# Kernel tuning notes

Hardware: AMD Instinct MI355X
Metric: run time of the kernel (lower is better)

## Reference

```python
import jax, jax.numpy as jnp
import numpy as np
from math import factorial

NODES = 40000      # number of nodes
EDGES = 640000     # number of edges (avg degree 16)
MUL = 8            # multiplicity of each irrep in hidden (8x0e+8x1e+8x2e)
NB = 16            # radial basis size (radial_neurons[0])
MAXR = 3.0         # max_radius
NSPECIES = 8
DEG = 16.0         # num_neighbors normalization
R8 = 1.0 / np.sqrt(8.0)

# ---------- real Clebsch-Gordan coefficients (precomputed with numpy) ----------
def _clebsch(j1, m1, j2, m2, j3, m3):
    f = factorial
    if m1 + m2 != m3:
        return 0.0
    pref = ((2*j3+1) * f(j3+j1-j2) * f(j3-j1+j2) * f(j1+j2-j3) / f(j1+j2+j3+1)) ** 0.5
    pref *= (f(j3+m3)*f(j3-m3)*f(j1-m1)*f(j1+m1)*f(j2-m2)*f(j2+m2)) ** 0.5
    lo = max(0, j2-j3-m1, j1-j3+m2)
    hi = min(j1+j2-j3, j1-m1, j2+m2)
    s = 0.0
    for k in range(lo, hi+1):
        s += (-1)**k / (f(k)*f(j1+j2-j3-k)*f(j1-m1-k)*f(j2+m2-k)*f(j3-j2+m1+k)*f(j3-j1-m2+k))
    return pref * s

def _U(l):
    # complex -> real spherical-harmonic change of basis (rows: real m, cols: complex m)
    U = np.zeros((2*l+1, 2*l+1), dtype=complex)
    s2 = 2 ** -0.5
    for m in range(-l, l+1):
        if m > 0:
            U[m+l, m+l] = (-1)**m * s2; U[m+l, -m+l] = s2
        elif m == 0:
            U[l, l] = 1.0
        else:
            U[m+l, m+l] = 1j*s2; U[m+l, -m+l] = -1j*((-1)**m)*s2
    return U

def _real_cg(l1, l2, l3):
    C = np.zeros((2*l1+1, 2*l2+1, 2*l3+1))
    for m1 in range(-l1, l1+1):
        for m2 in range(-l2, l2+1):
            m3 = m1 + m2
            if abs(m3) <= l3:
                C[m1+l1, m2+l2, m3+l3] = _clebsch(l1, m1, l2, m2, l3, m3)
    T = np.einsum('am,bn,co,mno->abc', _U(l1).conj(), _U(l2).conj(), _U(l3), C)
    R = T.imag if np.abs(T.imag).max() > np.abs(T.real).max() else T.real
    return jnp.asarray(R.astype(np.float32))

PATHS = [(0,0,0),(0,1,1),(0,2,2),(1,0,1),(1,1,0),(1,1,1),(1,1,2),
         (1,2,1),(1,2,2),(2,0,2),(2,1,1),(2,1,2),(2,2,0),(2,2,1),(2,2,2)]
CG = {p: _real_cg(*p) for p in PATHS}
NIN = {0: 3.0, 1: 6.0, 2: 6.0}  # fan-in path counts per output l in hidden convs

# ---------- irrep feature layout: [.., 72] = 8x0e | 8x1e | 8x2e ----------
def _split(h):
    lead = h.shape[:-1]
    return (h[..., :MUL],
            h[..., MUL:4*MUL].reshape(lead + (MUL, 3)),
            h[..., 4*MUL:].reshape(lead + (MUL, 5)))

def _merge(s, v, t):
    lead = s.shape[:-1]
    return jnp.concatenate([s, v.reshape(lead + (3*MUL,)), t.reshape(lead + (5*MUL,))], -1)

def _act(h):
    # e3nn Activation: silu on 0e scalars, identity on l>0
    s, v, t = _split(h)
    return _merge(jax.nn.silu(s), v, t)

def _radial(emb, w1, b1, w2, b2):
    return jax.nn.silu(emb @ w1 + b1) @ w2 + b2

def _sh(u):
    # component-normalized real spherical harmonics l=0,1,2 of unit vectors u [E,3]
    x, y, z = u[:, 0], u[:, 1], u[:, 2]
    c15 = np.sqrt(15.0); c5 = np.sqrt(5.0); c3 = np.sqrt(3.0)
    y1 = jnp.stack([y, z, x], -1) * c3
    y2 = jnp.stack([c15*x*y, c15*y*z, 0.5*c5*(3*z*z - 1.0), c15*x*z, 0.5*c15*(x*x - y*y)], -1)
    return jnp.concatenate([jnp.ones_like(x)[:, None], y1, y2], -1)

def _soft_onehot(r):
    # e3nn soft_one_hot_linspace, basis='smooth_finite', cutoff=True
    values = jnp.linspace(0.0, MAXR, NB + 2)[1:-1]
    step = MAXR / (NB + 1)
    d = (r[:, None] - values) / step
    inside = jnp.abs(d) < 1.0
    dd = jnp.where(inside, d, 0.0)
    f = jnp.exp(-1.0 / (1.0 + dd)) * jnp.exp(-1.0 / (1.0 - dd))
    return 1.14136 * np.exp(2.0) * jnp.where(inside, f, 0.0)

def _tp_first(hs, sh, w):
    # uvu TP: 8x0e (x) SH(1x0e+1x1e+1x2e) -> hidden; hs [E,8], sh [E,9], w [E,3,8]
    m_s = w[:, 0] * hs * sh[:, :1]
    m_v = w[:, 1][..., None] * hs[..., None] * sh[:, None, 1:4]
    m_t = w[:, 2][..., None] * hs[..., None] * sh[:, None, 4:9]
    return _merge(m_s, m_v, m_t)

def _tp_uuu(h1, h2, w):
    # depthwise (uuu) CG tensor product hidden (x) hidden -> hidden; w [E,15,8]
    s1, v1, t1 = _split(h1); s2, v2, t2 = _split(h2)
    a = {0: s1[..., None], 1: v1, 2: t1}
    b = {0: s2[..., None], 1: v2, 2: t2}
    out = {0: 0.0, 1: 0.0, 2: 0.0}
    for p, (l1, l2, l3) in enumerate(PATHS):
        out[l3] = out[l3] + w[:, p, :, None] * jnp.einsum('eci,ecj,ijk->eck', a[l1], b[l2], CG[(l1, l2, l3)])
    return _merge(out[0][..., 0] / np.sqrt(NIN[0]), out[1] / np.sqrt(NIN[1]), out[2] / np.sqrt(NIN[2]))

def _lin_hidden(h, lin):
    # irrep-wise linear self-connection, lin [3,8,8]
    s, v, t = _split(h)
    return _merge(s @ lin[0] * R8,
                  jnp.einsum('ncm,cd->ndm', v, lin[1]) * R8,
                  jnp.einsum('ncm,cd->ndm', t, lin[2]) * R8)

def _model(x, edge_index, edge_vec, embed_w, lin0, lin1, lin2, out_w,
           r0_w1, r0_b1, r0_w2, r0_b2, r1_w1, r1_b1, r1_w2, r1_b2,
           r2_w1, r2_b1, r2_w2, r2_b2):
    src, dst = edge_index[0], edge_index[1]
    h = embed_w[x]                                   # [N, 8] scalar node feats
    r = jnp.sqrt(jnp.sum(edge_vec**2, -1) + 1e-12)
    emb = _soft_onehot(r)                            # [E, 16]
    hb_sh = _sh(edge_vec / r[:, None])               # [E, 9]
    rdeg = 1.0 / np.sqrt(DEG)
    # conv 0 + activation
    w = _radial(emb, r0_w1, r0_b1, r0_w2, r0_b2).reshape(-1, 3, MUL)
    m = _tp_first(h[src], hb_sh, w)                  # [E, 72]
    agg = jax.ops.segment_sum(m, dst, num_segments=NODES) * rdeg
    h = _act(agg.at[:, :MUL].add((h @ lin0) * R8))
    hb = _act(m)
    # convs 1..2 + activation
    for (w1, b1, w2, b2, lin) in ((r1_w1, r1_b1, r1_w2, r1_b2, lin1),
                                  (r2_w1, r2_b1, r2_w2, r2_b2, lin2)):
        w = _radial(emb, w1, b1, w2, b2).reshape(-1, 15, MUL)
        m = _tp_uuu(h[src], hb, w)
        agg = jax.ops.segment_sum(m, dst, num_segments=NODES) * rdeg
        h = _act(_lin_hidden(h, lin) + agg)
        hb = _act(m)
    # output FullyConnectedTensorProduct(h, h) -> 8x0e (paths l(x)l->0)
    s, v, t = _split(h)
    i0 = s[:, :, None] * s[:, None, :]
    i1 = jnp.einsum('nim,njm->nij', v, v) / np.sqrt(3.0)
    i2 = jnp.einsum('nim,njm->nij', t, t) / np.sqrt(5.0)
    out = (jnp.einsum('nij,ijk->nk', i0, out_w[0])
           + jnp.einsum('nij,ijk->nk', i1, out_w[1])
           + jnp.einsum('nij,ijk->nk', i2, out_w[2])) / np.sqrt(3.0 * MUL * MUL)
    return out

def setup_inputs() -> dict:
    key = jax.random.key(0)
    ks = jax.random.split(key, 16)
    inp = {}
    inp['x'] = jax.random.randint(ks[0], (NODES,), 0, NSPECIES)
    inp['edge_index'] = jax.random.randint(ks[1], (2, EDGES), 0, NODES)
    inp['edge_vec'] = jax.random.normal(ks[2], (EDGES, 3), dtype=jnp.float32)
    inp['embed_w'] = jax.random.normal(ks[3], (NSPECIES, MUL), dtype=jnp.float32)
    inp['lin0'] = jax.random.normal(ks[4], (MUL, MUL), dtype=jnp.float32)
    inp['lin1'] = jax.random.normal(ks[5], (3, MUL, MUL), dtype=jnp.float32)
    inp['lin2'] = jax.random.normal(ks[6], (3, MUL, MUL), dtype=jnp.float32)
    inp['out_w'] = jax.random.normal(ks[7], (3, MUL, MUL, MUL), dtype=jnp.float32)
    for i, (name, od) in enumerate((('r0', 3*MUL), ('r1', 15*MUL), ('r2', 15*MUL))):
        k1, k2 = jax.random.split(ks[8+i])
        inp[name+'_w1'] = jax.random.normal(k1, (NB, 64), dtype=jnp.float32) / np.sqrt(NB)
        inp[name+'_b1'] = jnp.zeros((64,), dtype=jnp.float32)
        inp[name+'_w2'] = jax.random.normal(k2, (64, od), dtype=jnp.float32) / 8.0
        inp[name+'_b2'] = jnp.zeros((od,), dtype=jnp.float32)
    return inp

def reference(x, edge_index, edge_vec, embed_w, lin0, lin1, lin2, out_w,
              r0_w1, r0_b1, r0_w2, r0_b2, r1_w1, r1_b1, r1_w2, r1_b2,
              r2_w1, r2_b1, r2_w2, r2_b2):
    return _model(x, edge_index, edge_vec, embed_w, lin0, lin1, lin2, out_w,
                  r0_w1, r0_b1, r0_w2, r0_b2, r1_w1, r1_b1, r1_w2, r1_b2,
                  r2_w1, r2_b1, r2_w2, r2_b2)
```

## Files before the change

### kernel.cpp

```cpp
#include <hip/hip_runtime.h>

#define NODES 40000
#define EDGES 640000

typedef float f32x2v __attribute__((ext_vector_type(2)));
typedef float f32x4v __attribute__((ext_vector_type(4)));
typedef short short8v __attribute__((ext_vector_type(8)));

__device__ __forceinline__ float silu_f(float x) { return x / (1.0f + __expf(-x)); }
__device__ __forceinline__ f32x2v mk2(float a, float b) { f32x2v r; r[0] = a; r[1] = b; return r; }

__device__ __forceinline__ void tp_uuu2(const f32x2v* wv,
                                        f32x2v as, const f32x2v* av, const f32x2v* at,
                                        f32x2v bs, const f32x2v* bv, const f32x2v* bt,
                                        f32x2v& ms, f32x2v* mv, f32x2v* mt)
{
    const float CR = 0.70710678f;
    const float K1 = 0.31622777f;
    const float K3 = 0.54772256f;
    const float KA = 0.40824829f;
    const float KB = 0.70710678f;
    const float KC = 0.81649658f;
    const float L4 = 0.63245553f;
    const float G2 = 0.53452248f;
    const float G1 = 0.26726124f;
    const float HH = 0.46291005f;

    f32x2v os = {0.f, 0.f};
    f32x2v ov0 = {0.f, 0.f}, ov1 = {0.f, 0.f}, ov2 = {0.f, 0.f};
    f32x2v ot0 = {0.f, 0.f}, ot1 = {0.f, 0.f}, ot2 = {0.f, 0.f};
    f32x2v ot3 = {0.f, 0.f}, ot4 = {0.f, 0.f};

    os += wv[0] * as * bs;
    ov0 += wv[1] * as * bv[0]; ov1 += wv[1] * as * bv[1]; ov2 += wv[1] * as * bv[2];
    ot0 += wv[2] * as * bt[0]; ot1 += wv[2] * as * bt[1]; ot2 += wv[2] * as * bt[2];
    ot3 += wv[2] * as * bt[3]; ot4 += wv[2] * as * bt[4];
    ov0 += wv[3] * av[0] * bs; ov1 += wv[3] * av[1] * bs; ov2 += wv[3] * av[2] * bs;
    os += wv[4] * (-0.57735027f) * (av[0]*bv[0] + av[1]*bv[1] + av[2]*bv[2]);
    ov0 += wv[5] * CR * (av[1]*bv[2] - av[2]*bv[1]);
    ov1 += wv[5] * CR * (av[2]*bv[0] - av[0]*bv[2]);
    ov2 += wv[5] * CR * (av[0]*bv[1] - av[1]*bv[0]);
    ot0 += wv[6] * CR * (av[2]*bv[0] + av[0]*bv[2]);
    ot1 += wv[6] * CR * (av[0]*bv[1] + av[1]*bv[0]);
    ot2 += wv[6] * 0.40824829f * (2.f*av[1]*bv[1] - av[2]*bv[2] - av[0]*bv[0]);
    ot3 += wv[6] * CR * (av[2]*bv[1] + av[1]*bv[2]);
    ot4 += wv[6] * CR * (av[2]*bv[2] - av[0]*bv[0]);
    ov0 += wv[7] * (-K3*av[1]*bt[1] + K1*av[0]*bt[2] - K3*av[2]*bt[0] + K3*av[0]*bt[4]);
    ov1 += wv[7] * (-2.f*K1*av[1]*bt[2] - K3*av[2]*bt[3] - K3*av[0]*bt[1]);
    ov2 += wv[7] * (-K3*av[1]*bt[3] + K1*av[2]*bt[2] - K3*av[0]*bt[0] - K3*av[2]*bt[4]);
    ot0 += wv[8] * ( KC*av[1]*bt[4] - KA*av[2]*bt[3] + KA*av[0]*bt[1]);
    ot1 += wv[8] * ( KA*av[1]*bt[3] - KB*av[2]*bt[2] - KA*av[0]*bt[0] - KA*av[2]*bt[4]);
    ot2 += wv[8] * ( KB*av[2]*bt[1] - KB*av[0]*bt[3]);
    ot3 += wv[8] * (-KA*av[1]*bt[1] + KB*av[0]*bt[2] + KA*av[2]*bt[0] - KA*av[0]*bt[4]);
    ot4 += wv[8] * (-KC*av[1]*bt[0] + KA*av[2]*bt[1] + KA*av[0]*bt[3]);
    ot0 += wv[9] * at[0] * bs; ot1 += wv[9] * at[1] * bs; ot2 += wv[9] * at[2] * bs;
    ot3 += wv[9] * at[3] * bs; ot4 += wv[9] * at[4] * bs;
    ov0 += wv[10] * (-K3*bv[1]*at[1] + K1*bv[0]*at[2] - K3*bv[2]*at[0] + K3*bv[0]*at[4]);
    ov1 += wv[10] * (-2.f*K1*bv[1]*at[2] - K3*bv[2]*at[3] - K3*bv[0]*at[1]);
    ov2 += wv[10] * (-K3*bv[1]*at[3] + K1*bv[2]*at[2] - K3*bv[0]*at[0] - K3*bv[2]*at[4]);
    ot0 -= wv[11] * ( KC*bv[1]*at[4] - KA*bv[2]*at[3] + KA*bv[0]*at[1]);
    ot1 -= wv[11] * ( KA*bv[1]*at[3] - KB*bv[2]*at[2] - KA*bv[0]*at[0] - KA*bv[2]*at[4]);
    ot2 -= wv[11] * ( KB*bv[2]*at[1] - KB*bv[0]*at[3]);
    ot3 -= wv[11] * (-KA*bv[1]*at[1] + KB*bv[0]*at[2] + KA*bv[2]*at[0] - KA*bv[0]*at[4]);
    ot4 -= wv[11] * (-KC*bv[1]*at[0] + KA*bv[2]*at[1] + KA*bv[0]*at[3]);
    os += wv[12] * 0.44721360f * (at[0]*bt[0] + at[1]*bt[1] + at[2]*bt[2] + at[3]*bt[3] + at[4]*bt[4]);
    ov0 += wv[13] * ( K1*(at[0]*bt[1] - at[1]*bt[0]) + K3*(at[3]*bt[2] - at[2]*bt[3]) + K1*(at[4]*bt[3] - at[3]*bt[4]) );
    ov1 += wv[13] * ( L4*(at[0]*bt[4] - at[4]*bt[0]) + K1*(at[1]*bt[3] - at[3]*bt[1]) );
    ov2 += wv[13] * ( K1*(at[3]*bt[0] - at[0]*bt[3]) + K3*(at[2]*bt[1] - at[1]*bt[2]) + K1*(at[4]*bt[1] - at[1]*bt[4]) );
    ot0 += wv[14] * ( G2*(at[2]*bt[0] + at[0]*bt[2]) - HH*(at[1]*bt[3] + at[3]*bt[1]) );
    ot1 += wv[14] * (-HH*(at[3]*bt[0] + at[0]*bt[3]) + HH*(at[1]*bt[4] + at[4]*bt[1]) - G1*(at[2]*bt[1] + at[1]*bt[2]) );
    ot2 += wv[14] * ( G2*(at[0]*bt[0] + at[4]*bt[4] - at[2]*bt[2]) - G1*(at[1]*bt[1] + at[3]*bt[3]) );
    ot3 += wv[14] * (-HH*(at[1]*bt[0] + at[0]*bt[1]) - HH*(at[3]*bt[4] + at[4]*bt[3]) - G1*(at[2]*bt[3] + at[3]*bt[2]) );
    ot4 += wv[14] * ( G2*(at[2]*bt[4] + at[4]*bt[2]) + HH*(at[1]*bt[1] - at[3]*bt[3]) );

    ms = os * 0.57735027f;
    mv[0] = ov0 * 0.40824829f; mv[1] = ov1 * 0.40824829f; mv[2] = ov2 * 0.40824829f;
    mt[0] = ot0 * 0.40824829f; mt[1] = ot1 * 0.40824829f; mt[2] = ot2 * 0.40824829f;
    mt[3] = ot3 * 0.40824829f; mt[4] = ot4 * 0.40824829f;
}

__global__ void deg_kernel(const int* __restrict__ eidx, int* __restrict__ deg)
{
    int e = blockIdx.x * 256 + threadIdx.x;
    if (e < EDGES) atomicAdd(&deg[eidx[EDGES + e]], 1);
}

__launch_bounds__(1024)
__global__ void scan_kernel(const int* __restrict__ deg, int* __restrict__ off,
                            int* __restrict__ cursor)
{
    __shared__ int part[1024];
    const int t = threadIdx.x;
    const int base = t * 40;
    int v[40];
    if (t < 1000) {
        const int4* p4 = (const int4*)(deg + base);
        #pragma unroll
        for (int i = 0; i < 10; ++i) {
            int4 q = p4[i];
            v[4 * i + 0] = q.x; v[4 * i + 1] = q.y;
            v[4 * i + 2] = q.z; v[4 * i + 3] = q.w;
        }
    } else {
        #pragma unroll
        for (int i = 0; i < 40; ++i) v[i] = 0;
    }
    int loc[40];
    int s = 0;
    #pragma unroll
    for (int i = 0; i < 40; ++i) { loc[i] = s; s += v[i]; }
    part[t] = s;
    __syncthreads();
    for (int d = 1; d < 1024; d <<= 1) {
        int vv = (t >= d) ? part[t - d] : 0;
        __syncthreads();
        part[t] += vv;
        __syncthreads();
    }
    int tb = (t == 0) ? 0 : part[t - 1];
    if (t < 1000) {
        #pragma unroll
        for (int i = 0; i < 40; ++i) {
            off[base + i] = tb + loc[i];
            cursor[base + i] = tb + loc[i];
        }
    }
    if (t == 1023) off[NODES] = part[1023];
}

__global__ void build_kernel(const int* __restrict__ eidx, const float* __restrict__ ev,
                             int* __restrict__ cursor,
// ... 53 lines not shown
            float4 wb = *(const float4*)&w1[i * 64 + jb + 4];
            #pragma unroll
            for (int el = 0; el < 4; ++el) {
                float evv = emb_s[(egp * 4 + el) * 17 + i];
                acc2[el][0] += evv * wa.x; acc2[el][1] += evv * wa.y;
                acc2[el][2] += evv * wa.z; acc2[el][3] += evv * wa.w;
                acc2[el][4] += evv * wb.x; acc2[el][5] += evv * wb.y;
                acc2[el][6] += evv * wb.z; acc2[el][7] += evv * wb.w;
            }
        }
        #pragma unroll
        for (int el = 0; el < 4; ++el)
            #pragma unroll
            for (int k = 0; k < 8; ++k)
                hid_s[(egp * 4 + el) * 68 + jb + k] = silu_f(acc2[el][k]);
    }
    __syncthreads();

    const int c = tid & 7, g = (tid >> 3) & 7, wv_ = tid >> 6;
    float wacc[3][4];
    #pragma unroll
    for (int p = 0; p < 3; ++p) {
        float bb = b2[p * 8 + c];
        #pragma unroll
        for (int q = 0; q < 4; ++q) wacc[p][q] = bb;
    }
    for (int jb = 0; jb < 64; jb += 4) {
        float4 h4[4];
        #pragma unroll
        for (int q = 0; q < 4; ++q)
            h4[q] = *(const float4*)&hid_s[(wv_ * 32 + q * 8 + g) * 68 + jb];
        #pragma unroll
        for (int p = 0; p < 3; ++p) {
            float4 w4 = *(const float4*)&w2t[(p * 8 + c) * 68 + jb];
            #pragma unroll
            for (int q = 0; q < 4; ++q)
                wacc[p][q] += h4[q].x * w4.x + h4[q].y * w4.y + h4[q].z * w4.z + h4[q].w * w4.w;
        }
    }

    const int ebase = wv_ * 32 + g;
    #pragma unroll
    for (int q = 0; q < 4; ++q) {
        const int sl = e0 + ebase + 8 * q;
        const int sn = (int)((unsigned)srcs[sl] & 0xffffu);
        float hs = embw[xs[sn] * 8 + c];
        float* me = mbuf + (size_t)sl * 72;
        me[c]      = wacc[0][q] * hs;
        me[8 + c]  = wacc[1][q] * hs;
        me[16 + c] = wacc[2][q] * hs;
    }
}

__launch_bounds__(256, 3)
__global__ void tp_edge(const float* __restrict__ evp, const int* __restrict__ srcs,
                        const float* __restrict__ h,
                        const float* __restrict__ w1, const float* __restrict__ b1,
                        const float* __restrict__ w2, const float* __restrict__ b2,
                        float* __restrict__ mbuf, float* __restrict__ agg,
                        const int writeM, const int compactB)
{
    __shared__ float ws_t[120 * 68];
    __shared__ unsigned short hid_s[128 * 64];
    __shared__ int dst_s[66];
    float* emb_s = ws_t;

    const int tid = threadIdx.x;
    const int e0 = blockIdx.x * 128;

    for (int idx = tid; idx < 2048; idx += 256) {
        int e = idx >> 4, i = idx & 15;
        const float* ep = evp + (size_t)(e0 + e) * 3;
        float ex = ep[0], ey = ep[1], ez = ep[2];
        float r = sqrtf(ex * ex + ey * ey + ez * ez + 1e-12f);
        float d = r * (17.0f / 3.0f) - (float)(i + 1);
        float f = 0.0f;
        if (fabsf(d) < 1.0f) f = 8.433572869f * __expf(-2.0f / (1.0f - d * d));
        emb_s[e * 17 + i] = f;
    }
    __syncthreads();

    {
        const int egp = tid >> 3;
        const int jb = (tid & 7) * 8;
        f32x2v acc2[2][8];
        #pragma unroll
        for (int pr = 0; pr < 2; ++pr)
            #pragma unroll
            for (int k = 0; k < 8; ++k) { float bb = b1[jb + k]; acc2[pr][k] = mk2(bb, bb); }
        #pragma unroll
        for (int i = 0; i < 16; ++i) {
            float4 wa = *(const float4*)&w1[i * 64 + jb];
            float4 wb = *(const float4*)&w1[i * 64 + jb + 4];
            #pragma unroll
            for (int pr = 0; pr < 2; ++pr) {
                f32x2v evv = mk2(emb_s[(egp * 4 + 2 * pr) * 17 + i],
                                 emb_s[(egp * 4 + 2 * pr + 1) * 17 + i]);
                acc2[pr][0] += evv * wa.x; acc2[pr][1] += evv * wa.y;
                acc2[pr][2] += evv * wa.z; acc2[pr][3] += evv * wa.w;
                acc2[pr][4] += evv * wb.x; acc2[pr][5] += evv * wb.y;
                acc2[pr][6] += evv * wb.z; acc2[pr][7] += evv * wb.w;
            }
        }
        #pragma unroll
        for (int pr = 0; pr < 2; ++pr) {
            #pragma unroll
            for (int u = 0; u < 2; ++u) {
                unsigned int us[8];
                #pragma unroll
                for (int k = 0; k < 8; ++k) {
                    unsigned int b = __float_as_uint(silu_f(acc2[pr][k][u]));
                    b += 0x7fffu + ((b >> 16) & 1u);
                    us[k] = b >> 16;
                }
                uint4 pk;
                pk.x = us[0] | (us[1] << 16);
                pk.y = us[2] | (us[3] << 16);
                pk.z = us[4] | (us[5] << 16);
                pk.w = us[6] | (us[7] << 16);
                int rr = egp * 4 + 2 * pr + u;
                *(uint4*)&hid_s[rr * 64 + (jb ^ ((rr & 7) << 3))] = pk;
            }
        }
    }
    __syncthreads();

    const int l  = tid & 63;
    const int wq = tid >> 6;
    const int lr = l & 15;
    const int lg = l >> 4;

    short8v bhi[2][2], blo[2][2];
    #pragma unroll
    for (int n2 = 0; n2 < 2; ++n2) {
        int col  = (2 * wq + n2) * 16 + lr;
        int colc = col < 120 ? col : 119;
        #pragma unroll
        for (int ks = 0; ks < 2; ++ks) {
            short8v hv, lv;
            #pragma unroll
            for (int j = 0; j < 8; ++j) {
                int k = ks * 32 + lg * 8 + j;
                float v = w2[k * 120 + colc];
                if (col >= 120) v = 0.0f;
                unsigned bb = __float_as_uint(v);
                unsigned rh = bb + 0x7fffu + ((bb >> 16) & 1u);
                float hf = __uint_as_float((rh >> 16) << 16);
                unsigned bl = __float_as_uint(v - hf);
                bl += 0x7fffu + ((bl >> 16) & 1u);
                hv[j] = (short)(rh >> 16);
                lv[j] = (short)(bl >> 16);
            }
            bhi[n2][ks] = hv;
            blo[n2][ks] = lv;
        }
    }

    const int c = tid & 7, g = (tid >> 3) & 7, wv_ = tid >> 6;
    const int ebh = wv_ * 16 + g;

    #pragma unroll
    for (int half = 0; half < 2; ++half) {
        #pragma unroll
        for (int mm = 0; mm < 4; ++mm) {
            int e  = 64 * half + 16 * mm + lr;
            int sw = (e & 7) << 3;
            short8v a0 = *(const short8v*)&hid_s[e * 64 + ((lg * 8) ^ sw)];
            short8v a1 = *(const short8v*)&hid_s[e * 64 + ((32 + lg * 8) ^ sw)];
            #pragma unroll
            for (int n2 = 0; n2 < 2; ++n2) {
                int col = (2 * wq + n2) * 16 + lr;
                float bias = (col < 120) ? b2[col] : 0.0f;
                f32x4v acc;
                acc[0] = bias; acc[1] = bias; acc[2] = bias; acc[3] = bias;
                acc = __builtin_amdgcn_mfma_f32_16x16x32_bf16(a0, bhi[n2][0], acc, 0, 0, 0);
                acc = __builtin_amdgcn_mfma_f32_16x16x32_bf16(a1, bhi[n2][1], acc, 0, 0, 0);
                acc = __builtin_amdgcn_mfma_f32_16x16x32_bf16(a0, blo[n2][0], acc, 0, 0, 0);
                acc = __builtin_amdgcn_mfma_f32_16x16x32_bf16(a1, blo[n2][1], acc, 0, 0, 0);
                if (col < 120)
                    *(f32x4v*)&ws_t[col * 68 + 16 * mm + lg * 4] = acc;
            }
        }
        __syncthreads();

        {
            const int eA = e0 + 64 * half + ebh;
            const int eB = eA + 8;
            const unsigned pkA = (unsigned)srcs[eA], pkB = (unsigned)srcs[eB];
            const int snA = (int)(pkA & 0xffffu), snB = (int)(pkB & 0xffffu);
            const float* hn0 = h + (size_t)snA * 72 + c * 9;
            const float* hn1 = h + (size_t)snB * 72 + c * 9;

            f32x2v as = mk2(hn0[0], hn1[0]);
            f32x2v av[3], at[5], bv[3], bt[5], bs;
            #pragma unroll
            for (int i = 0; i < 3; ++i) av[i] = mk2(hn0[1 + i], hn1[1 + i]);
            #pragma unroll
            for (int i = 0; i < 5; ++i) at[i] = mk2(hn0[4 + i], hn1[4 + i]);

            if (compactB) {
                float w0A = mbuf[(size_t)eA * 72 + c];
                float w1A = mbuf[(size_t)eA * 72 + 8 + c];
                float w2A = mbuf[(size_t)eA * 72 + 16 + c];
                float w0B = mbuf[(size_t)eB * 72 + c];
                float w1B = mbuf[(size_t)eB * 72 + 8 + c];
                float w2B = mbuf[(size_t)eB * 72 + 16 + c];
                const float* epA = evp + (size_t)eA * 3;
                const float* epB = evp + (size_t)eB * 3;
                float exA = epA[0], eyA = epA[1], ezA = epA[2];
                float exB = epB[0], eyB = epB[1], ezB = epB[2];
                float rA = sqrtf(exA * exA + eyA * eyA + ezA * ezA + 1e-12f);
                float rB = sqrtf(exB * exB + eyB * eyB + ezB * ezB + 1e-12f);
                float iA = 1.0f / rA, iB = 1.0f / rB;
                float xA = exA * iA, yA = eyA * iA, zA = ezA * iA;
                float xB = exB * iB, yB = eyB * iB, zB = ezB * iB;
                const float c3 = 1.7320508f, c15 = 3.8729833f, c5 = 2.2360680f;
                bs = mk2(silu_f(w0A), silu_f(w0B));
                bv[0] = mk2(w1A * (c3 * yA), w1B * (c3 * yB));
                bv[1] = mk2(w1A * (c3 * zA), w1B * (c3 * zB));
                bv[2] = mk2(w1A * (c3 * xA), w1B * (c3 * xB));
                bt[0] = mk2(w2A * (c15 * xA * yA), w2B * (c15 * xB * yB));
                bt[1] = mk2(w2A * (c15 * yA * zA), w2B * (c15 * yB * zB));
                bt[2] = mk2(w2A * (0.5f * c5 * (3.f * zA * zA - 1.f)),
                            w2B * (0.5f * c5 * (3.f * zB * zB - 1.f)));
                bt[3] = mk2(w2A * (c15 * xA * zA), w2B * (c15 * xB * zB));
                bt[4] = mk2(w2A * (0.5f * c15 * (xA * xA - yA * yA)),
                            w2B * (0.5f * c15 * (xB * xB - yB * yB)));
            } else {
                const float* me0 = mbuf + (size_t)eA * 72 + c * 9;
                const float* me1 = mbuf + (size_t)eB * 72 + c * 9;
                bs = mk2(silu_f(me0[0]), silu_f(me1[0]));
                #pragma unroll
                for (int i = 0; i < 3; ++i) bv[i] = mk2(me0[1 + i], me1[1 + i]);
                #pragma unroll
                for (int i = 0; i < 5; ++i) bt[i] = mk2(me0[4 + i], me1[4 + i]);
            }

            f32x2v wvv[15];
            #pragma unroll
            for (int p = 0; p < 15; ++p)
                wvv[p] = mk2(ws_t[(p * 8 + c) * 68 + ebh],
                             ws_t[(p * 8 + c) * 68 + ebh + 8]);

            f32x2v ms, mv[3], mt[5];
            tp_uuu2(wvv, as, av, at, bs, bv, bt, ms, mv, mt);

            if (writeM) {
                float* mo0 = mbuf + (size_t)eA * 72 + c * 9;
                float* mo1 = mbuf + (size_t)eB * 72 + c * 9;
                mo0[0] = ms[0]; mo1[0] = ms[1];
                #pragma unroll
                for (int i = 0; i < 3; ++i) { mo0[1 + i] = mv[i][0]; mo1[1 + i] = mv[i][1]; }
                #pragma unroll
                for (int i = 0; i < 5; ++i) { mo0[4 + i] = mt[i][0]; mo1[4 + i] = mt[i][1]; }
            }

            if (tid <= 64) {
                int gs = e0 + 64 * half + tid;
                dst_s[tid] = (gs < EDGES) ? (int)((unsigned)srcs[gs] >> 16) : -1;
            }
            __syncthreads();

            float* m_s = ws_t;
            const int lA = ebh, lB = ebh + 8;
            m_s[lA * 72 + c * 9] = ms[0]; m_s[lB * 72 + c * 9] = ms[1];
            #pragma unroll
            for (int i = 0; i < 3; ++i) {
                m_s[lA * 72 + c * 9 + 1 + i] = mv[i][0];
                m_s[lB * 72 + c * 9 + 1 + i] = mv[i][1];
            }
            #pragma unroll
            for (int i = 0; i < 5; ++i) {
                m_s[lA * 72 + c * 9 + 4 + i] = mt[i][0];
                m_s[lB * 72 + c * 9 + 4 + i] = mt[i][1];
            }
            __syncthreads();

            if (tid < 216) {
                const int seg  = tid / 72;
                const int comp = tid - seg * 72;
                const int p0 = (seg == 0) ? 0  : ((seg == 1) ? 22 : 43);
                const int p1 = (seg == 0) ? 22 : ((seg == 1) ? 43 : 64);
                float sum = 0.f;
                int cur = dst_s[p0];
                for (int p = p0; p < p1; ++p) {
                    sum += m_s[p * 72 + comp];
                    int nxt = dst_s[p + 1];
                    if (nxt != cur) {
                        atomicAdd(&agg[(size_t)cur * 72 + comp], sum);
                        sum = 0.f; cur = nxt;
                    }
                }
                if (cur >= 0) atomicAdd(&agg[(size_t)cur * 72 + comp], sum);
            }
        }
        if (half == 0) __syncthreads();
    }
}

__global__ void node0(const int* __restrict__ xs, const float* __restrict__ embw,
                      const float* __restrict__ lin0, const float* __restrict__ mbuf,
                      const float* __restrict__ evp,
                      const int* __restrict__ off, float* __restrict__ h)
{
    int idx = blockIdx.x * 256 + threadIdx.x;
    int n = idx >> 3, c = idx & 7;
    int xb = xs[n] * 8;
    float dot = 0.f;
    #pragma unroll
    for (int d = 0; d < 8; ++d) dot += embw[xb + d] * lin0[d * 8 + c];

    float an[9];
    #pragma unroll
    for (int i = 0; i < 9; ++i) an[i] = 0.f;
    const float c3 = 1.7320508f, c15 = 3.8729833f, c5 = 2.2360680f;
    const int beg = off[n], end = off[n + 1];
    for (int p = beg; p < end; ++p) {
        float w0 = mbuf[(size_t)p * 72 + c];
        float w1 = mbuf[(size_t)p * 72 + 8 + c];
        float w2 = mbuf[(size_t)p * 72 + 16 + c];
        const float* ep = evp + (size_t)p * 3;
        float ex = ep[0], ey = ep[1], ez = ep[2];
        float r = sqrtf(ex * ex + ey * ey + ez * ez + 1e-12f);
        float inv = 1.0f / r;
        float x = ex * inv, y = ey * inv, z = ez * inv;
        an[0] += w0;
        an[1] += w1 * (c3 * y);
        an[2] += w1 * (c3 * z);
        an[3] += w1 * (c3 * x);
        an[4] += w2 * (c15 * x * y);
        an[5] += w2 * (c15 * y * z);
        an[6] += w2 * (0.5f * c5 * (3.f * z * z - 1.f));
        an[7] += w2 * (c15 * x * z);
        an[8] += w2 * (0.5f * c15 * (x * x - y * y));
    }

    float* hn = h + (size_t)n * 72 + c * 9;
    hn[0] = silu_f(an[0] * 0.25f + dot * 0.35355339f);
    #pragma unroll
    for (int i = 1; i < 9; ++i) hn[i] = an[i] * 0.25f;
}

__global__ void node12(const float* __restrict__ hin, const float* __restrict__ lin,
                       const float* __restrict__ agg, float* __restrict__ hout)
{
    int idx = blockIdx.x * 256 + threadIdx.x;
    int n = idx >> 3, d = idx & 7;

    float an[9];
// ... 145 lines not shown
```

Measured before the change: 666.4 us.

## Split radial weight GEMM into two column halves to shrink LDS and raise occupancy

The radial MLP output (120 columns) is now computed in two 64-column halves. Tensor-product paths 0-7 are evaluated on the first half before the second half overwrites the same smaller shared buffer, and paths 8-14 then run on the second half. This shrinks the shared weight tile from 120x68 to 64x72 floats so the launch bound can rise from 3 to 4 blocks per CU. The cost is two extra block barriers per half-iteration and partial accumulators that stay live across the split, which adds register pressure.

```diff
diff --git a/kernel.cpp b/kernel.cpp
--- a/kernel.cpp
+++ b/kernel.cpp
@@ -10,12 +10,39 @@
 __device__ __forceinline__ float silu_f(float x) { return x / (1.0f + __expf(-x)); }
 __device__ __forceinline__ f32x2v mk2(float a, float b) { f32x2v r; r[0] = a; r[1] = b; return r; }
 
-__device__ __forceinline__ void tp_uuu2(const f32x2v* wv,
-                                        f32x2v as, const f32x2v* av, const f32x2v* at,
-                                        f32x2v bs, const f32x2v* bv, const f32x2v* bt,
-                                        f32x2v& ms, f32x2v* mv, f32x2v* mt)
+__device__ __forceinline__ void tp_paths07(const f32x2v* wv,
+        f32x2v as, const f32x2v* av, const f32x2v* at,
+        f32x2v bs, const f32x2v* bv, const f32x2v* bt,
+        f32x2v& os, f32x2v* ov, f32x2v* ot)
 {
     const float CR = 0.70710678f;
+    const float K1 = 0.31622777f;
+    const float K3 = 0.54772256f;
+
+    os += wv[0] * as * bs;
+    ov[0] += wv[1] * as * bv[0]; ov[1] += wv[1] * as * bv[1]; ov[2] += wv[1] * as * bv[2];
+    ot[0] += wv[2] * as * bt[0]; ot[1] += wv[2] * as * bt[1]; ot[2] += wv[2] * as * bt[2];
+    ot[3] += wv[2] * as * bt[3]; ot[4] += wv[2] * as * bt[4];
+    ov[0] += wv[3] * av[0] * bs; ov[1] += wv[3] * av[1] * bs; ov[2] += wv[3] * av[2] * bs;
+    os += wv[4] * (-0.57735027f) * (av[0]*bv[0] + av[1]*bv[1] + av[2]*bv[2]);
+    ov[0] += wv[5] * CR * (av[1]*bv[2] - av[2]*bv[1]);
+    ov[1] += wv[5] * CR * (av[2]*bv[0] - av[0]*bv[2]);
+    ov[2] += wv[5] * CR * (av[0]*bv[1] - av[1]*bv[0]);
+    ot[0] += wv[6] * CR * (av[2]*bv[0] + av[0]*bv[2]);
+    ot[1] += wv[6] * CR * (av[0]*bv[1] + av[1]*bv[0]);
+    ot[2] += wv[6] * 0.40824829f * (2.f*av[1]*bv[1] - av[2]*bv[2] - av[0]*bv[0]);
+    ot[3] += wv[6] * CR * (av[2]*bv[1] + av[1]*bv[2]);
+    ot[4] += wv[6] * CR * (av[2]*bv[2] - av[0]*bv[0]);
+    ov[0] += wv[7] * (-K3*av[1]*bt[1] + K1*av[0]*bt[2] - K3*av[2]*bt[0] + K3*av[0]*bt[4]);
+    ov[1] += wv[7] * (-2.f*K1*av[1]*bt[2] - K3*av[2]*bt[3] - K3*av[0]*bt[1]);
+    ov[2] += wv[7] * (-K3*av[1]*bt[3] + K1*av[2]*bt[2] - K3*av[0]*bt[0] - K3*av[2]*bt[4]);
+}
+
+__device__ __forceinline__ void tp_paths814(const f32x2v* wv,
+        const f32x2v* av, const f32x2v* at,
+        f32x2v bs, const f32x2v* bv, const f32x2v* bt,
+        f32x2v& os, f32x2v* ov, f32x2v* ot)
+{
     const float K1 = 0.31622777f;
     const float K3 = 0.54772256f;
     const float KA = 0.40824829f;
@@ -26,57 +53,30 @@
     const float G1 = 0.26726124f;
     const float HH = 0.46291005f;
 
-    f32x2v os = {0.f, 0.f};
-    f32x2v ov0 = {0.f, 0.f}, ov1 = {0.f, 0.f}, ov2 = {0.f, 0.f};
-    f32x2v ot0 = {0.f, 0.f}, ot1 = {0.f, 0.f}, ot2 = {0.f, 0.f};
-    f32x2v ot3 = {0.f, 0.f}, ot4 = {0.f, 0.f};
-
-    os += wv[0] * as * bs;
-    ov0 += wv[1] * as * bv[0]; ov1 += wv[1] * as * bv[1]; ov2 += wv[1] * as * bv[2];
-    ot0 += wv[2] * as * bt[0]; ot1 += wv[2] * as * bt[1]; ot2 += wv[2] * as * bt[2];
-    ot3 += wv[2] * as * bt[3]; ot4 += wv[2] * as * bt[4];
-    ov0 += wv[3] * av[0] * bs; ov1 += wv[3] * av[1] * bs; ov2 += wv[3] * av[2] * bs;
-    os += wv[4] * (-0.57735027f) * (av[0]*bv[0] + av[1]*bv[1] + av[2]*bv[2]);
-    ov0 += wv[5] * CR * (av[1]*bv[2] - av[2]*bv[1]);
-    ov1 += wv[5] * CR * (av[2]*bv[0] - av[0]*bv[2]);
-    ov2 += wv[5] * CR * (av[0]*bv[1] - av[1]*bv[0]);
-    ot0 += wv[6] * CR * (av[2]*bv[0] + av[0]*bv[2]);
-    ot1 += wv[6] * CR * (av[0]*bv[1] + av[1]*bv[0]);
-    ot2 += wv[6] * 0.40824829f * (2.f*av[1]*bv[1] - av[2]*bv[2] - av[0]*bv[0]);
-    ot3 += wv[6] * CR * (av[2]*bv[1] + av[1]*bv[2]);
-    ot4 += wv[6] * CR * (av[2]*bv[2] - av[0]*bv[0]);
-    ov0 += wv[7] * (-K3*av[1]*bt[1] + K1*av[0]*bt[2] - K3*av[2]*bt[0] + K3*av[0]*bt[4]);
-    ov1 += wv[7] * (-2.f*K1*av[1]*bt[2] - K3*av[2]*bt[3] - K3*av[0]*bt[1]);
-    ov2 += wv[7] * (-K3*av[1]*bt[3] + K1*av[2]*bt[2] - K3*av[0]*bt[0] - K3*av[2]*bt[4]);
-    ot0 += wv[8] * ( KC*av[1]*bt[4] - KA*av[2]*bt[3] + KA*av[0]*bt[1]);
-    ot1 += wv[8] * ( KA*av[1]*bt[3] - KB*av[2]*bt[2] - KA*av[0]*bt[0] - KA*av[2]*bt[4]);
-    ot2 += wv[8] * ( KB*av[2]*bt[1] - KB*av[0]*bt[3]);
-    ot3 += wv[8] * (-KA*av[1]*bt[1] + KB*av[0]*bt[2] + KA*av[2]*bt[0] - KA*av[0]*bt[4]);
-    ot4 += wv[8] * (-KC*av[1]*bt[0] + KA*av[2]*bt[1] + KA*av[0]*bt[3]);
-    ot0 += wv[9] * at[0] * bs; ot1 += wv[9] * at[1] * bs; ot2 += wv[9] * at[2] * bs;
-    ot3 += wv[9] * at[3] * bs; ot4 += wv[9] * at[4] * bs;
-    ov0 += wv[10] * (-K3*bv[1]*at[1] + K1*bv[0]*at[2] - K3*bv[2]*at[0] + K3*bv[0]*at[4]);
-    ov1 += wv[10] * (-2.f*K1*bv[1]*at[2] - K3*bv[2]*at[3] - K3*bv[0]*at[1]);
-    ov2 += wv[10] * (-K3*bv[1]*at[3] + K1*bv[2]*at[2] - K3*bv[0]*at[0] - K3*bv[2]*at[4]);
-    ot0 -= wv[11] * ( KC*bv[1]*at[4] - KA*bv[2]*at[3] + KA*bv[0]*at[1]);
-    ot1 -= wv[11] * ( KA*bv[1]*at[3] - KB*bv[2]*at[2] - KA*bv[0]*at[0] - KA*bv[2]*at[4]);
-    ot2 -= wv[11] * ( KB*bv[2]*at[1] - KB*bv[0]*at[3]);
-    ot3 -= wv[11] * (-KA*bv[1]*at[1] + KB*bv[0]*at[2] + KA*bv[2]*at[0] - KA*bv[0]*at[4]);
-    ot4 -= wv[11] * (-KC*bv[1]*at[0] + KA*bv[2]*at[1] + KA*bv[0]*at[3]);
-    os += wv[12] * 0.44721360f * (at[0]*bt[0] + at[1]*bt[1] + at[2]*bt[2] + at[3]*bt[3] + at[4]*bt[4]);
-    ov0 += wv[13] * ( K1*(at[0]*bt[1] - at[1]*bt[0]) + K3*(at[3]*bt[2] - at[2]*bt[3]) + K1*(at[4]*bt[3] - at[3]*bt[4]) );
-    ov1 += wv[13] * ( L4*(at[0]*bt[4] - at[4]*bt[0]) + K1*(at[1]*bt[3] - at[3]*bt[1]) );
-    ov2 += wv[13] * ( K1*(at[3]*bt[0] - at[0]*bt[3]) + K3*(at[2]*bt[1] - at[1]*bt[2]) + K1*(at[4]*bt[1] - at[1]*bt[4]) );
-    ot0 += wv[14] * ( G2*(at[2]*bt[0] + at[0]*bt[2]) - HH*(at[1]*bt[3] + at[3]*bt[1]) );
-    ot1 += wv[14] * (-HH*(at[3]*bt[0] + at[0]*bt[3]) + HH*(at[1]*bt[4] + at[4]*bt[1]) - G1*(at[2]*bt[1] + at[1]*bt[2]) );
-    ot2 += wv[14] * ( G2*(at[0]*bt[0] + at[4]*bt[4] - at[2]*bt[2]) - G1*(at[1]*bt[1] + at[3]*bt[3]) );
-    ot3 += wv[14] * (-HH*(at[1]*bt[0] + at[0]*bt[1]) - HH*(at[3]*bt[4] + at[4]*bt[3]) - G1*(at[2]*bt[3] + at[3]*bt[2]) );
-    ot4 += wv[14] * ( G2*(at[2]*bt[4] + at[4]*bt[2]) + HH*(at[1]*bt[1] - at[3]*bt[3]) );
-
-    ms = os * 0.57735027f;
-    mv[0] = ov0 * 0.40824829f; mv[1] = ov1 * 0.40824829f; mv[2] = ov2 * 0.40824829f;
-    mt[0] = ot0 * 0.40824829f; mt[1] = ot1 * 0.40824829f; mt[2] = ot2 * 0.40824829f;
-    mt[3] = ot3 * 0.40824829f; mt[4] = ot4 * 0.40824829f;
+    ot[0] += wv[0] * ( KC*av[1]*bt[4] - KA*av[2]*bt[3] + KA*av[0]*bt[1]);
+    ot[1] += wv[0] * ( KA*av[1]*bt[3] - KB*av[2]*bt[2] - KA*av[0]*bt[0] - KA*av[2]*bt[4]);
+    ot[2] += wv[0] * ( KB*av[2]*bt[1] - KB*av[0]*bt[3]);
+    ot[3] += wv[0] * (-KA*av[1]*bt[1] + KB*av[0]*bt[2] + KA*av[2]*bt[0] - KA*av[0]*bt[4]);
+    ot[4] += wv[0] * (-KC*av[1]*bt[0] + KA*av[2]*bt[1] + KA*av[0]*bt[3]);
+    ot[0] += wv[1] * at[0] * bs; ot[1] += wv[1] * at[1] * bs; ot[2] += wv[1] * at[2] * bs;
+    ot[3] += wv[1] * at[3] * bs; ot[4] += wv[1] * at[4] * bs;
+    ov[0] += wv[2] * (-K3*bv[1]*at[1] + K1*bv[0]*at[2] - K3*bv[2]*at[0] + K3*bv[0]*at[4]);
+    ov[1] += wv[2] * (-2.f*K1*bv[1]*at[2] - K3*bv[2]*at[3] - K3*bv[0]*at[1]);
+    ov[2] += wv[2] * (-K3*bv[1]*at[3] + K1*bv[2]*at[2] - K3*bv[0]*at[0] - K3*bv[2]*at[4]);
+    ot[0] -= wv[3] * ( KC*bv[1]*at[4] - KA*bv[2]*at[3] + KA*bv[0]*at[1]);
+    ot[1] -= wv[3] * ( KA*bv[1]*at[3] - KB*bv[2]*at[2] - KA*bv[0]*at[0] - KA*bv[2]*at[4]);
+    ot[2] -= wv[3] * ( KB*bv[2]*at[1] - KB*bv[0]*at[3]);
+    ot[3] -= wv[3] * (-KA*bv[1]*at[1] + KB*bv[0]*at[2] + KA*bv[2]*at[0] - KA*bv[0]*at[4]);
+    ot[4] -= wv[3] * (-KC*bv[1]*at[0] + KA*bv[2]*at[1] + KA*bv[0]*at[3]);
+    os += wv[4] * 0.44721360f * (at[0]*bt[0] + at[1]*bt[1] + at[2]*bt[2] + at[3]*bt[3] + at[4]*bt[4]);
+    ov[0] += wv[5] * ( K1*(at[0]*bt[1] - at[1]*bt[0]) + K3*(at[3]*bt[2] - at[2]*bt[3]) + K1*(at[4]*bt[3] - at[3]*bt[4]) );
+    ov[1] += wv[5] * ( L4*(at[0]*bt[4] - at[4]*bt[0]) + K1*(at[1]*bt[3] - at[3]*bt[1]) );
+    ov[2] += wv[5] * ( K1*(at[3]*bt[0] - at[0]*bt[3]) + K3*(at[2]*bt[1] - at[1]*bt[2]) + K1*(at[4]*bt[1] - at[1]*bt[4]) );
+    ot[0] += wv[6] * ( G2*(at[2]*bt[0] + at[0]*bt[2]) - HH*(at[1]*bt[3] + at[3]*bt[1]) );
+    ot[1] += wv[6] * (-HH*(at[3]*bt[0] + at[0]*bt[3]) + HH*(at[1]*bt[4] + at[4]*bt[1]) - G1*(at[2]*bt[1] + at[1]*bt[2]) );
+    ot[2] += wv[6] * ( G2*(at[0]*bt[0] + at[4]*bt[4] - at[2]*bt[2]) - G1*(at[1]*bt[1] + at[3]*bt[3]) );
+    ot[3] += wv[6] * (-HH*(at[1]*bt[0] + at[0]*bt[1]) - HH*(at[3]*bt[4] + at[4]*bt[3]) - G1*(at[2]*bt[3] + at[3]*bt[2]) );
+    ot[4] += wv[6] * ( G2*(at[2]*bt[4] + at[4]*bt[2]) + HH*(at[1]*bt[1] - at[3]*bt[3]) );
 }
 
 __global__ void deg_kernel(const int* __restrict__ eidx, int* __restrict__ deg)
@@ -236,7 +236,7 @@
     }
 }
 
-__launch_bounds__(256, 3)
+__launch_bounds__(256, 4)
 __global__ void tp_edge(const float* __restrict__ evp, const int* __restrict__ srcs,
                         const float* __restrict__ h,
                         const float* __restrict__ w1, const float* __restrict__ b1,
@@ -244,7 +244,7 @@
                         float* __restrict__ mbuf, float* __restrict__ agg,
                         const int writeM, const int compactB)
 {
-    __shared__ float ws_t[120 * 68];
+    __shared__ float ws_t[64 * 72];
     __shared__ unsigned short hid_s[128 * 64];
     __shared__ int dst_s[66];
     float* emb_s = ws_t;
@@ -316,8 +316,8 @@
 
     short8v bhi[2][2], blo[2][2];
     #pragma unroll
-    for (int n2 = 0; n2 < 2; ++n2) {
-        int col  = (2 * wq + n2) * 16 + lr;
+    for (int sub = 0; sub < 2; ++sub) {
+        int col  = 64 * sub + wq * 16 + lr;
         int colc = col < 120 ? col : 119;
         #pragma unroll
         for (int ks = 0; ks < 2; ++ks) {
@@ -335,8 +335,8 @@
                 hv[j] = (short)(rh >> 16);
                 lv[j] = (short)(bl >> 16);
             }
-            bhi[n2][ks] = hv;
-            blo[n2][ks] = lv;
+            bhi[sub][ks] = hv;
+            blo[sub][ks] = lv;
         }
     }
 
@@ -351,32 +351,28 @@
             int sw = (e & 7) << 3;
             short8v a0 = *(const short8v*)&hid_s[e * 64 + ((lg * 8) ^ sw)];
             short8v a1 = *(const short8v*)&hid_s[e * 64 + ((32 + lg * 8) ^ sw)];
-            #pragma unroll
-            for (int n2 = 0; n2 < 2; ++n2) {
-                int col = (2 * wq + n2) * 16 + lr;
-                float bias = (col < 120) ? b2[col] : 0.0f;
-                f32x4v acc;
-                acc[0] = bias; acc[1] = bias; acc[2] = bias; acc[3] = bias;
-                acc = __builtin_amdgcn_mfma_f32_16x16x32_bf16(a0, bhi[n2][0], acc, 0, 0, 0);
-                acc = __builtin_amdgcn_mfma_f32_16x16x32_bf16(a1, bhi[n2][1], acc, 0, 0, 0);
-                acc = __builtin_amdgcn_mfma_f32_16x16x32_bf16(a0, blo[n2][0], acc, 0, 0, 0);
-                acc = __builtin_amdgcn_mfma_f32_16x16x32_bf16(a1, blo[n2][1], acc, 0, 0, 0);
-                if (col < 120)
-                    *(f32x4v*)&ws_t[col * 68 + 16 * mm + lg * 4] = acc;
-            }
+            int col = wq * 16 + lr;
+            float bias = b2[col];
+            f32x4v acc;
+            acc[0] = bias; acc[1] = bias; acc[2] = bias; acc[3] = bias;
+            acc = __builtin_amdgcn_mfma_f32_16x16x32_bf16(a0, bhi[0][0], acc, 0, 0, 0);
+            acc = __builtin_amdgcn_mfma_f32_16x16x32_bf16(a1, bhi[0][1], acc, 0, 0, 0);
+            acc = __builtin_amdgcn_mfma_f32_16x16x32_bf16(a0, blo[0][0], acc, 0, 0, 0);
+            acc = __builtin_amdgcn_mfma_f32_16x16x32_bf16(a1, blo[0][1], acc, 0, 0, 0);
+            *(f32x4v*)&ws_t[col * 72 + 16 * mm + lg * 4] = acc;
         }
         __syncthreads();
 
+        const int eA = e0 + 64 * half + ebh;
+        const int eB = eA + 8;
+        f32x2v as, av[3], at[5], bs, bv[3], bt[5];
+        f32x2v os, ov[3], ot[5];
         {
-            const int eA = e0 + 64 * half + ebh;
-            const int eB = eA + 8;
             const unsigned pkA = (unsigned)srcs[eA], pkB = (unsigned)srcs[eB];
             const int snA = (int)(pkA & 0xffffu), snB = (int)(pkB & 0xffffu);
             const float* hn0 = h + (size_t)snA * 72 + c * 9;
             const float* hn1 = h + (size_t)snB * 72 + c * 9;
-
-            f32x2v as = mk2(hn0[0], hn1[0]);
-            f32x2v av[3], at[5], bv[3], bt[5], bs;
+            as = mk2(hn0[0], hn1[0]);
             #pragma unroll
             for (int i = 0; i < 3; ++i) av[i] = mk2(hn0[1 + i], hn1[1 + i]);
             #pragma unroll
@@ -420,14 +416,54 @@
                 for (int i = 0; i < 5; ++i) bt[i] = mk2(me0[4 + i], me1[4 + i]);
             }
 
-            f32x2v wvv[15];
-            #pragma unroll
-            for (int p = 0; p < 15; ++p)
-                wvv[p] = mk2(ws_t[(p * 8 + c) * 68 + ebh],
-                             ws_t[(p * 8 + c) * 68 + ebh + 8]);
-
-            f32x2v ms, mv[3], mt[5];
-            tp_uuu2(wvv, as, av, at, bs, bv, bt, ms, mv, mt);
+            os = mk2(0.f, 0.f);
+            #pragma unroll
+            for (int i = 0; i < 3; ++i) ov[i] = mk2(0.f, 0.f);
+            #pragma unroll
+            for (int i = 0; i < 5; ++i) ot[i] = mk2(0.f, 0.f);
+
+            f32x2v wvv[8];
+            #pragma unroll
+            for (int p = 0; p < 8; ++p)
+                wvv[p] = mk2(ws_t[(p * 8 + c) * 72 + ebh],
+                             ws_t[(p * 8 + c) * 72 + ebh + 8]);
+            tp_paths07(wvv, as, av, at, bs, bv, bt, os, ov, ot);
+        }
+        __syncthreads();
+
+        #pragma unroll
+        for (int mm = 0; mm < 4; ++mm) {
+            int e  = 64 * half + 16 * mm + lr;
+            int sw = (e & 7) << 3;
+            short8v a0 = *(const short8v*)&hid_s[e * 64 + ((lg * 8) ^ sw)];
+            short8v a1 = *(const short8v*)&hid_s[e * 64 + ((32 + lg * 8) ^ sw)];
+            int col = 64 + wq * 16 + lr;
+            float bias = (col < 120) ? b2[col] : 0.0f;
+            f32x4v acc;
+            acc[0] = bias; acc[1] = bias; acc[2] = bias; acc[3] = bias;
+            acc = __builtin_amdgcn_mfma_f32_16x16x32_bf16(a0, bhi[1][0], acc, 0, 0, 0);
+            acc = __builtin_amdgcn_mfma_f32_16x16x32_bf16(a1, bhi[1][1], acc, 0, 0, 0);
+            acc = __builtin_amdgcn_mfma_f32_16x16x32_bf16(a0, blo[1][0], acc, 0, 0, 0);
+            acc = __builtin_amdgcn_mfma_f32_16x16x32_bf16(a1, blo[1][1], acc, 0, 0, 0);
+            if (col < 120)
+                *(f32x4v*)&ws_t[(col - 64) * 72 + 16 * mm + lg * 4] = acc;
+        }
+        __syncthreads();
+
+        f32x2v ms, mv[3], mt[5];
+        {
+            f32x2v wvv[7];
+            #pragma unroll
+            for (int p = 0; p < 7; ++p)
+                wvv[p] = mk2(ws_t[(p * 8 + c) * 72 + ebh],
+                             ws_t[(p * 8 + c) * 72 + ebh + 8]);
+            tp_paths814(wvv, av, at, bs, bv, bt, os, ov, ot);
+
+            ms = os * 0.57735027f;
+            #pragma unroll
+            for (int i = 0; i < 3; ++i) mv[i] = ov[i] * 0.40824829f;
+            #pragma unroll
+            for (int i = 0; i < 5; ++i) mt[i] = ot[i] * 0.40824829f;
 
             if (writeM) {
                 float* mo0 = mbuf + (size_t)eA * 72 + c * 9;
@@ -438,45 +474,45 @@
                 #pragma unroll
                 for (int i = 0; i < 5; ++i) { mo0[4 + i] = mt[i][0]; mo1[4 + i] = mt[i][1]; }
             }
-
-            if (tid <= 64) {
-                int gs = e0 + 64 * half + tid;
-                dst_s[tid] = (gs < EDGES) ? (int)((unsigned)srcs[gs] >> 16) : -1;
+        }
+
+        if (tid <= 64) {
+            int gs = e0 + 64 * half + tid;
+            dst_s[tid] = (gs < EDGES) ? (int)((unsigned)srcs[gs] >> 16) : -1;
+        }
+        __syncthreads();
+
+        float* m_s = ws_t;
+        const int lA = ebh, lB = ebh + 8;
+        m_s[lA * 72 + c * 9] = ms[0]; m_s[lB * 72 + c * 9] = ms[1];
+        #pragma unroll
+        for (int i = 0; i < 3; ++i) {
+            m_s[lA * 72 + c * 9 + 1 + i] = mv[i][0];
+            m_s[lB * 72 + c * 9 + 1 + i] = mv[i][1];
+        }
+        #pragma unroll
+        for (int i = 0; i < 5; ++i) {
+            m_s[lA * 72 + c * 9 + 4 + i] = mt[i][0];
+            m_s[lB * 72 + c * 9 + 4 + i] = mt[i][1];
+        }
+        __syncthreads();
+
+        if (tid < 216) {
+            const int seg  = tid / 72;
+            const int comp = tid - seg * 72;
+            const int p0 = (seg == 0) ? 0  : ((seg == 1) ? 22 : 43);
+            const int p1 = (seg == 0) ? 22 : ((seg == 1) ? 43 : 64);
+            float sum = 0.f;
+            int cur = dst_s[p0];
+            for (int p = p0; p < p1; ++p) {
+                sum += m_s[p * 72 + comp];
+                int nxt = dst_s[p + 1];
+                if (nxt != cur) {
+                    atomicAdd(&agg[(size_t)cur * 72 + comp], sum);
+                    sum = 0.f; cur = nxt;
+                }
             }
-            __syncthreads();
-
-            float* m_s = ws_t;
-            const int lA = ebh, lB = ebh + 8;
-            m_s[lA * 72 + c * 9] = ms[0]; m_s[lB * 72 + c * 9] = ms[1];
-            #pragma unroll
-            for (int i = 0; i < 3; ++i) {
-                m_s[lA * 72 + c * 9 + 1 + i] = mv[i][0];
-                m_s[lB * 72 + c * 9 + 1 + i] = mv[i][1];
-            }
-            #pragma unroll
-            for (int i = 0; i < 5; ++i) {
-                m_s[lA * 72 + c * 9 + 4 + i] = mt[i][0];
-                m_s[lB * 72 + c * 9 + 4 + i] = mt[i][1];
-            }
-            __syncthreads();
-
-            if (tid < 216) {
-                const int seg  = tid / 72;
-                const int comp = tid - seg * 72;
-                const int p0 = (seg == 0) ? 0  : ((seg == 1) ? 22 : 43);
-                const int p1 = (seg == 0) ? 22 : ((seg == 1) ? 43 : 64);
-                float sum = 0.f;
-                int cur = dst_s[p0];
-                for (int p = p0; p < p1; ++p) {
-                    sum += m_s[p * 72 + comp];
-                    int nxt = dst_s[p + 1];
-                    if (nxt != cur) {
-                        atomicAdd(&agg[(size_t)cur * 72 + comp], sum);
-                        sum = 0.f; cur = nxt;
-                    }
-                }
-                if (cur >= 0) atomicAdd(&agg[(size_t)cur * 72 + comp], sum);
-            }
+            if (cur >= 0) atomicAdd(&agg[(size_t)cur * 72 + comp], sum);
         }
         if (half == 0) __syncthreads();
     }
```

After: 676.0 us. Within noise of the previous version (+1.4%).

## Compute radial MLP hidden per half to shrink LDS and raise occupancy

Applied to the files above, without the earlier changes.

Moves the radial basis embedding and first MLP layer inside the per-half loop, so only 64 edges of bf16 hidden activations are staged at a time. This halves hid_s and moves dst_s into the reused ws_t buffer, reducing LDS per block, and raises launch_bounds min blocks from 3 to 4. The aim is more resident blocks per CU to hide memory latency. The cost is extra barriers per half, an un-unrolled half loop, and tighter register limits that may cause spills.

```diff
diff --git a/kernel.cpp b/kernel.cpp
--- a/kernel.cpp
+++ b/kernel.cpp
@@ -236,7 +236,7 @@
     }
 }
 
-__launch_bounds__(256, 3)
+__launch_bounds__(256, 4)
 __global__ void tp_edge(const float* __restrict__ evp, const int* __restrict__ srcs,
                         const float* __restrict__ h,
                         const float* __restrict__ w1, const float* __restrict__ b1,
@@ -245,69 +245,12 @@
                         const int writeM, const int compactB)
 {
     __shared__ float ws_t[120 * 68];
-    __shared__ unsigned short hid_s[128 * 64];
-    __shared__ int dst_s[66];
+    __shared__ unsigned short hid_s[64 * 64];
     float* emb_s = ws_t;
+    int* dst_s = (int*)&ws_t[4864];
 
     const int tid = threadIdx.x;
     const int e0 = blockIdx.x * 128;
-
-    for (int idx = tid; idx < 2048; idx += 256) {
-        int e = idx >> 4, i = idx & 15;
-        const float* ep = evp + (size_t)(e0 + e) * 3;
-        float ex = ep[0], ey = ep[1], ez = ep[2];
-        float r = sqrtf(ex * ex + ey * ey + ez * ez + 1e-12f);
-        float d = r * (17.0f / 3.0f) - (float)(i + 1);
-        float f = 0.0f;
-        if (fabsf(d) < 1.0f) f = 8.433572869f * __expf(-2.0f / (1.0f - d * d));
-        emb_s[e * 17 + i] = f;
-    }
-    __syncthreads();
-
-    {
-        const int egp = tid >> 3;
-        const int jb = (tid & 7) * 8;
-        f32x2v acc2[2][8];
-        #pragma unroll
-        for (int pr = 0; pr < 2; ++pr)
-            #pragma unroll
-            for (int k = 0; k < 8; ++k) { float bb = b1[jb + k]; acc2[pr][k] = mk2(bb, bb); }
-        #pragma unroll
-        for (int i = 0; i < 16; ++i) {
-            float4 wa = *(const float4*)&w1[i * 64 + jb];
-            float4 wb = *(const float4*)&w1[i * 64 + jb + 4];
-            #pragma unroll
-            for (int pr = 0; pr < 2; ++pr) {
-                f32x2v evv = mk2(emb_s[(egp * 4 + 2 * pr) * 17 + i],
-                                 emb_s[(egp * 4 + 2 * pr + 1) * 17 + i]);
-                acc2[pr][0] += evv * wa.x; acc2[pr][1] += evv * wa.y;
-                acc2[pr][2] += evv * wa.z; acc2[pr][3] += evv * wa.w;
-                acc2[pr][4] += evv * wb.x; acc2[pr][5] += evv * wb.y;
-                acc2[pr][6] += evv * wb.z; acc2[pr][7] += evv * wb.w;
-            }
-        }
-        #pragma unroll
-        for (int pr = 0; pr < 2; ++pr) {
-            #pragma unroll
-            for (int u = 0; u < 2; ++u) {
-                unsigned int us[8];
-                #pragma unroll
-                for (int k = 0; k < 8; ++k) {
-                    unsigned int b = __float_as_uint(silu_f(acc2[pr][k][u]));
-                    b += 0x7fffu + ((b >> 16) & 1u);
-                    us[k] = b >> 16;
-                }
-                uint4 pk;
-                pk.x = us[0] | (us[1] << 16);
-                pk.y = us[2] | (us[3] << 16);
-                pk.z = us[4] | (us[5] << 16);
-                pk.w = us[6] | (us[7] << 16);
-                int rr = egp * 4 + 2 * pr + u;
-                *(uint4*)&hid_s[rr * 64 + (jb ^ ((rr & 7) << 3))] = pk;
-            }
-        }
-    }
-    __syncthreads();
 
     const int l  = tid & 63;
     const int wq = tid >> 6;
@@ -343,11 +286,61 @@
     const int c = tid & 7, g = (tid >> 3) & 7, wv_ = tid >> 6;
     const int ebh = wv_ * 16 + g;
 
-    #pragma unroll
     for (int half = 0; half < 2; ++half) {
+        const int eh0 = e0 + 64 * half;
+
+        for (int idx = tid; idx < 1024; idx += 256) {
+            int e = idx >> 4, i = idx & 15;
+            const float* ep = evp + (size_t)(eh0 + e) * 3;
+            float ex = ep[0], ey = ep[1], ez = ep[2];
+            float r = sqrtf(ex * ex + ey * ey + ez * ez + 1e-12f);
+            float d = r * (17.0f / 3.0f) - (float)(i + 1);
+            float f = 0.0f;
+            if (fabsf(d) < 1.0f) f = 8.433572869f * __expf(-2.0f / (1.0f - d * d));
+            emb_s[e * 17 + i] = f;
+        }
+        __syncthreads();
+
+        {
+            const int egp = tid >> 3;
+            const int jb = (tid & 7) * 8;
+            f32x2v acc2[8];
+            #pragma unroll
+            for (int k = 0; k < 8; ++k) { float bb = b1[jb + k]; acc2[k] = mk2(bb, bb); }
+            #pragma unroll
+            for (int i = 0; i < 16; ++i) {
+                float4 wa = *(const float4*)&w1[i * 64 + jb];
+                float4 wb = *(const float4*)&w1[i * 64 + jb + 4];
+                f32x2v evv = mk2(emb_s[(egp * 2) * 17 + i],
+                                 emb_s[(egp * 2 + 1) * 17 + i]);
+                acc2[0] += evv * wa.x; acc2[1] += evv * wa.y;
+                acc2[2] += evv * wa.z; acc2[3] += evv * wa.w;
+                acc2[4] += evv * wb.x; acc2[5] += evv * wb.y;
+                acc2[6] += evv * wb.z; acc2[7] += evv * wb.w;
+            }
+            #pragma unroll
+            for (int u = 0; u < 2; ++u) {
+                unsigned int us[8];
+                #pragma unroll
+                for (int k = 0; k < 8; ++k) {
+                    unsigned int b = __float_as_uint(silu_f(acc2[k][u]));
+                    b += 0x7fffu + ((b >> 16) & 1u);
+                    us[k] = b >> 16;
+                }
+                uint4 pk;
+                pk.x = us[0] | (us[1] << 16);
+                pk.y = us[2] | (us[3] << 16);
+                pk.z = us[4] | (us[5] << 16);
+                pk.w = us[6] | (us[7] << 16);
+                int rr = egp * 2 + u;
+                *(uint4*)&hid_s[rr * 64 + (jb ^ ((rr & 7) << 3))] = pk;
+            }
+        }
+        __syncthreads();
+
         #pragma unroll
         for (int mm = 0; mm < 4; ++mm) {
-            int e  = 64 * half + 16 * mm + lr;
+            int e  = 16 * mm + lr;
             int sw = (e & 7) << 3;
             short8v a0 = *(const short8v*)&hid_s[e * 64 + ((lg * 8) ^ sw)];
             short8v a1 = *(const short8v*)&hid_s[e * 64 + ((32 + lg * 8) ^ sw)];
@@ -367,8 +360,9 @@
         }
         __syncthreads();
 
+        f32x2v ms, mv[3], mt[5];
         {
-            const int eA = e0 + 64 * half + ebh;
+            const int eA = eh0 + ebh;
             const int eB = eA + 8;
             const unsigned pkA = (unsigned)srcs[eA], pkB = (unsigned)srcs[eB];
             const int snA = (int)(pkA & 0xffffu), snB = (int)(pkB & 0xffffu);
@@ -426,7 +420,6 @@
                 wvv[p] = mk2(ws_t[(p * 8 + c) * 68 + ebh],
                              ws_t[(p * 8 + c) * 68 + ebh + 8]);
 
-            f32x2v ms, mv[3], mt[5];
             tp_uuu2(wvv, as, av, at, bs, bv, bt, ms, mv, mt);
 
             if (writeM) {
@@ -438,13 +431,10 @@
                 #pragma unroll
                 for (int i = 0; i < 5; ++i) { mo0[4 + i] = mt[i][0]; mo1[4 + i] = mt[i][1]; }
             }
-
-            if (tid <= 64) {
-                int gs = e0 + 64 * half + tid;
-                dst_s[tid] = (gs < EDGES) ? (int)((unsigned)srcs[gs] >> 16) : -1;
-            }
-            __syncthreads();
-
+        }
+        __syncthreads();
+
+        {
             float* m_s = ws_t;
             const int lA = ebh, lB = ebh + 8;
             m_s[lA * 72 + c * 9] = ms[0]; m_s[lB * 72 + c * 9] = ms[1];
@@ -458,27 +448,32 @@
                 m_s[lA * 72 + c * 9 + 4 + i] = mt[i][0];
                 m_s[lB * 72 + c * 9 + 4 + i] = mt[i][1];
             }
-            __syncthreads();
-
-            if (tid < 216) {
-                const int seg  = tid / 72;
-                const int comp = tid - seg * 72;
-                const int p0 = (seg == 0) ? 0  : ((seg == 1) ? 22 : 43);
-                const int p1 = (seg == 0) ? 22 : ((seg == 1) ? 43 : 64);
-                float sum = 0.f;
-                int cur = dst_s[p0];
-                for (int p = p0; p < p1; ++p) {
-                    sum += m_s[p * 72 + comp];
-                    int nxt = dst_s[p + 1];
-                    if (nxt != cur) {
-                        atomicAdd(&agg[(size_t)cur * 72 + comp], sum);
-                        sum = 0.f; cur = nxt;
-                    }
+            if (tid <= 64) {
+                int gs = eh0 + tid;
+                dst_s[tid] = (gs < EDGES) ? (int)((unsigned)srcs[gs] >> 16) : -1;
+            }
+        }
+        __syncthreads();
+
+        if (tid < 216) {
+            const int seg  = tid / 72;
+            const int comp = tid - seg * 72;
+            const int p0 = (seg == 0) ? 0  : ((seg == 1) ? 22 : 43);
+            const int p1 = (seg == 0) ? 22 : ((seg == 1) ? 43 : 64);
+            float sum = 0.f;
+            int cur = dst_s[p0];
+            const float* m_s = ws_t;
+            for (int p = p0; p < p1; ++p) {
+                sum += m_s[p * 72 + comp];
+                int nxt = dst_s[p + 1];
+                if (nxt != cur) {
+                    atomicAdd(&agg[(size_t)cur * 72 + comp], sum);
+                    sum = 0.f; cur = nxt;
                 }
-                if (cur >= 0) atomicAdd(&agg[(size_t)cur * 72 + comp], sum);
-            }
-        }
-        if (half == 0) __syncthreads();
+            }
+            if (cur >= 0) atomicAdd(&agg[(size_t)cur * 72 + comp], sum);
+        }
+        __syncthreads();
     }
 }
 
```

New measurement: 2.663 ms. +299.6%, slower.
